# Performance work log

Measured on AMD Instinct MI355X. Metric: run time of the kernel, lower is better.

The kernel has to match this reference:

```python
import jax, jax.numpy as jnp
import numpy as np


def setup_inputs() -> dict:
    key = jax.random.key(0)
    k1, k2, k3 = jax.random.split(key, 3)
    B, H, S, D = 2, 16, 2048, 64
    q = jax.random.normal(k1, (B, H, S, D), dtype=jnp.float32)
    k = jax.random.normal(k2, (B, H, S, D), dtype=jnp.float32)
    v = jax.random.normal(k3, (B, H, S, D), dtype=jnp.float32)
    return {"q": q, "k": k, "v": v}


def reference(q, k, v):
    # q,k,v: [B,H,S,D]; causal attention with 1/sqrt(D) scaling, fp32 softmax.
    scale = 1.0 / (q.shape[-1] ** 0.5)
    scores = jnp.einsum('bhqd,bhkd->bhqk', q * scale, k)  # [B,H,S,S]
    S = scores.shape[-1]
    causal_mask = jnp.triu(jnp.ones((S, S), dtype=bool), k=1)
    scores = jnp.where(causal_mask, -jnp.inf, scores)
    attn = jax.nn.softmax(scores.astype(jnp.float32), axis=-1).astype(q.dtype)
    output = jnp.einsum('bhqk,bhkd->bhqd', attn, v)
    # Module also returns an all-zeros attn_weights placeholder of shape [B,H,S,S]
    attn_weights = jnp.zeros(scores.shape, dtype=q.dtype)
    return (output, attn_weights)
```

## Files before the change

### kernel.cpp

```cpp
#include <hip/hip_runtime.h>


typedef __bf16 bf16x8 __attribute__((ext_vector_type(8)));
typedef float f32x4 __attribute__((ext_vector_type(4)));

#define LOG2E 1.44269504088896340736f

__device__ __forceinline__ unsigned short f2bf(float f) {
  unsigned int u = __float_as_uint(f);
  u += 0x7fffu + ((u >> 16) & 1u);
  return (unsigned short)(u >> 16);
}

__device__ __forceinline__ void block_sync_lds() {
  asm volatile("s_waitcnt lgkmcnt(0)" ::: "memory");
  __builtin_amdgcn_s_barrier();
}

__device__ __forceinline__ float redmax_q(float x) {
  float a = x, b = x;
  asm volatile("" : "+v"(b));
  asm("v_permlane16_swap_b32 %0, %1" : "+v"(a), "+v"(b));
  float m = fmaxf(a, b);
  float c = m, d = m;
  asm volatile("" : "+v"(d));
  asm("v_permlane32_swap_b32 %0, %1" : "+v"(c), "+v"(d));
  return fmaxf(c, d);
}
__device__ __forceinline__ float redsum_q(float x) {
  float a = x, b = x;
  asm volatile("" : "+v"(b));
  asm("v_permlane16_swap_b32 %0, %1" : "+v"(a), "+v"(b));
  float s = a + b;
  float c = s, d = s;
  asm volatile("" : "+v"(d));
  asm("v_permlane32_swap_b32 %0, %1" : "+v"(c), "+v"(d));
  return c + d;
}

constexpr int Sdim = 2048, Ddim = 64, BHn = 32;
constexpr int STiles = 16;
constexpr int LDK = 72;
constexpr int OUT0 = BHn * Sdim * Ddim;
constexpr size_t FILL_PER_BH = 1048576;

__device__ __forceinline__ int vswz_m(int d) { return ((d >> 2) ^ (d >> 5)) & 7; }
__device__ __forceinline__ int vrow(int d) { return (d & 56) | ((d ^ (d >> 3)) & 7); }

__global__ __launch_bounds__(256, 2)
void flash_causal_kernel(const float* __restrict__ Q, const float* __restrict__ K,
                         const float* __restrict__ V, float* __restrict__ out) {
  __shared__ unsigned short Klds[2][64 * LDK];
  __shared__ unsigned short Vlds[2][64 * LDK];
  __shared__ unsigned short Plds[4][2][16 * LDK];

  const int tid  = threadIdx.x;
  const int wave = tid >> 6;
  const int lane = tid & 63;
  const int quad = lane >> 4;
  const int l15  = lane & 15;

  const int bh = blockIdx.x & (BHn - 1);
  const int g  = (int)(blockIdx.x >> 5);
  const int s  = (g & 1) ? (STiles - 1) - (g >> 1) : (g >> 1);
  const int jmax = 2 * s + 1;

  const int base  = bh * Sdim * Ddim;
  const int qbase = s * 128;

  bf16x8 aq[2][2];
  #pragma unroll
  for (int f = 0; f < 2; ++f) {
    const float* qp = Q + base + (qbase + 64 * f + wave * 16 + l15) * Ddim + quad * 8;
    #pragma unroll
    for (int s2 = 0; s2 < 2; ++s2) {
      float4 a = *(const float4*)(qp + 32 * s2);
      float4 b = *(const float4*)(qp + 32 * s2 + 4);
      union { unsigned short u[8]; bf16x8 v; } u;
      u.u[0] = f2bf(a.x * 0.125f); u.u[1] = f2bf(a.y * 0.125f);
      u.u[2] = f2bf(a.z * 0.125f); u.u[3] = f2bf(a.w * 0.125f);
      u.u[4] = f2bf(b.x * 0.125f); u.u[5] = f2bf(b.y * 0.125f);
      u.u[6] = f2bf(b.z * 0.125f); u.u[7] = f2bf(b.w * 0.125f);
      aq[f][s2] = u.v;
    }
  }

  f32x4 ot[2][4];
  #pragma unroll
  for (int f = 0; f < 2; ++f)
    #pragma unroll
    for (int t = 0; t < 4; ++t) ot[f][t] = (f32x4){0.f, 0.f, 0.f, 0.f};
  float mrun[2] = {-__builtin_inff(), -__builtin_inff()};
  float lrun[2] = {0.f, 0.f};

  const float4* kg4 = (const float4*)(K + base);
  const float4* vg4 = (const float4*)(V + base);
  float4 kf[4], vf[4];

  auto ldtile = [&](int j) {
    const float4* kp = kg4 + j * 1024;
    const float4* vp = vg4 + j * 1024;
    #pragma unroll
    for (int i = 0; i < 4; ++i) { kf[i] = kp[i * 256 + tid]; vf[i] = vp[i * 256 + tid]; }
  };
  auto stage = [&](int buf) {
    #pragma unroll
    for (int i = 0; i < 4; ++i) {
      int lin = i * 256 + tid;
      int row = lin >> 4;
      int c4  = (lin & 15) << 2;
      uint2 t2;
      t2.x = (unsigned int)f2bf(kf[i].x) | ((unsigned int)f2bf(kf[i].y) << 16);
      t2.y = (unsigned int)f2bf(kf[i].z) | ((unsigned int)f2bf(kf[i].w) << 16);
      *(uint2*)&Klds[buf][row * LDK + c4] = t2;
      const int sw = vswz_m(c4) << 3;
      Vlds[buf][vrow(c4 + 0) * LDK + (row ^ sw)] = f2bf(vf[i].x);
      Vlds[buf][vrow(c4 + 1) * LDK + (row ^ sw)] = f2bf(vf[i].y);
      Vlds[buf][vrow(c4 + 2) * LDK + (row ^ sw)] = f2bf(vf[i].z);
      Vlds[buf][vrow(c4 + 3) * LDK + (row ^ sw)] = f2bf(vf[i].w);
    }
  };

  ldtile(0); stage(0); ldtile(1);

  for (int j = 0; j <= jmax; ++j) {
    block_sync_lds();
    if (j < jmax) stage((j + 1) & 1);
    if (j + 2 <= jmax) ldtile(j + 2);

    const unsigned short* Kb = Klds[j & 1];
    const unsigned short* Vb = Vlds[j & 1];
    const bool f0act = (j <= 2 * s);

    f32x4 sc[2][4];
    #pragma unroll
    for (int f = 0; f < 2; ++f)
      #pragma unroll
      for (int t = 0; t < 4; ++t) sc[f][t] = (f32x4){0.f, 0.f, 0.f, 0.f};
    __builtin_amdgcn_s_setprio(1);
    #pragma unroll
    for (int s2 = 0; s2 < 2; ++s2) {
      #pragma unroll
      for (int t = 0; t < 4; ++t) {
        bf16x8 ka = *(const bf16x8*)&Kb[(16 * t + l15) * LDK + 32 * s2 + quad * 8];
        sc[0][t] = __builtin_amdgcn_mfma_f32_16x16x32_bf16(ka, aq[0][s2], sc[0][t], 0, 0, 0);
        sc[1][t] = __builtin_amdgcn_mfma_f32_16x16x32_bf16(ka, aq[1][s2], sc[1][t], 0, 0, 0);
      }
    }
    __builtin_amdgcn_s_setprio(0);

    #pragma unroll
    for (int f = 0; f < 2; ++f) {
      if (j == 2 * s + f) {
        const int qml = wave * 16 + l15;
        #pragma unroll
        for (int t = 0; t < 4; ++t)
          #pragma unroll
          for (int r = 0; r < 4; ++r)
            if (16 * t + 4 * quad + r > qml) sc[f][t][r] = -__builtin_inff();
      }
    }

    #pragma unroll
    for (int f = 0; f < 2; ++f) {
      if (f == 0 && !f0act) continue;
      float tmx[4];
      #pragma unroll
      for (int t = 0; t < 4; ++t)
        tmx[t] = fmaxf(fmaxf(sc[f][t][0], sc[f][t][1]),
                       fmaxf(sc[f][t][2], sc[f][t][3]));
      float mx = fmaxf(fmaxf(tmx[0], tmx[1]), fmaxf(tmx[2], tmx[3]));
      mx = redmax_q(mx);
      float mn    = fmaxf(mrun[f], mx);
      float alpha = __builtin_amdgcn_exp2f((mrun[f] - mn) * LOG2E);
      float msc   = mn * LOG2E;
      mrun[f] = mn;
      float rsp[4];
      #pragma unroll
      for (int t = 0; t < 4; ++t) {
        float p0 = __builtin_amdgcn_exp2f(fmaf(sc[f][t][0], LOG2E, -msc));
        float p1 = __builtin_amdgcn_exp2f(fmaf(sc[f][t][1], LOG2E, -msc));
        float p2 = __builtin_amdgcn_exp2f(fmaf(sc[f][t][2], LOG2E, -msc));
        float p3 = __builtin_amdgcn_exp2f(fmaf(sc[f][t][3], LOG2E, -msc));
        sc[f][t][0] = p0; sc[f][t][1] = p1; sc[f][t][2] = p2; sc[f][t][3] = p3;
        rsp[t] = (p0 + p1) + (p2 + p3);
      }
      float rs = (rsp[0] + rsp[1]) + (rsp[2] + rsp[3]);
      rs = redsum_q(rs);
      lrun[f] = lrun[f] * alpha + rs;
      #pragma unroll
      for (int t = 0; t < 4; ++t) {
        uint2 pw;
        pw.x = (unsigned int)f2bf(sc[f][t][0]) | ((unsigned int)f2bf(sc[f][t][1]) << 16);
        pw.y = (unsigned int)f2bf(sc[f][t][2]) | ((unsigned int)f2bf(sc[f][t][3]) << 16);
        *(uint2*)&Plds[wave][f][l15 * LDK + 16 * t + 4 * quad] = pw;
      }
      #pragma unroll
      for (int t = 0; t < 4; ++t)
        #pragma unroll
        for (int r = 0; r < 4; ++r) ot[f][t][r] *= alpha;
    }

    __builtin_amdgcn_s_setprio(1);
    #pragma unroll
    for (int s2 = 0; s2 < 2; ++s2) {
      bf16x8 pb0, pb1;
      if (f0act) pb0 = *(const bf16x8*)&Plds[wave][0][l15 * LDK + 32 * s2 + quad * 8];
      pb1 = *(const bf16x8*)&Plds[wave][1][l15 * LDK + 32 * s2 + quad * 8];
      #pragma unroll
      for (int t = 0; t < 4; ++t) {
        const int d = 16 * t + l15;
        bf16x8 va = *(const bf16x8*)&Vb[vrow(d) * LDK + (((4 * s2 + quad) ^ vswz_m(d)) << 3)];
        if (f0act)
          ot[0][t] = __builtin_amdgcn_mfma_f32_16x16x32_bf16(va, pb0, ot[0][t], 0, 0, 0);
        ot[1][t] = __builtin_amdgcn_mfma_f32_16x16x32_bf16(va, pb1, ot[1][t], 0, 0, 0);
      }
    }
    __builtin_amdgcn_s_setprio(0);
  }

  #pragma unroll
  for (int f = 0; f < 2; ++f) {
    float inv = 1.0f / lrun[f];
    float* orow = out + base + (qbase + 64 * f + wave * 16 + l15) * Ddim + 4 * quad;
    #pragma unroll
    for (int t = 0; t < 4; ++t) {
      f32x4 o4;
      o4.x = ot[f][t][0] * inv; o4.y = ot[f][t][1] * inv;
      o4.z = ot[f][t][2] * inv; o4.w = ot[f][t][3] * inv;
      *(f32x4*)(orow + 16 * t) = o4;
    }
  }

  {
    const int gp = (STiles - 1) - s;
    const int w  = 2 * gp + 1;
    const size_t start_f4 = (size_t)bh * FILL_PER_BH + (size_t)4096 * (gp * gp);
    const size_t count_f4 = (size_t)4096 * w;
    f32x4 z4 = (f32x4){0.f, 0.f, 0.f, 0.f};
    f32x4* zp = (f32x4*)(out + OUT0) + start_f4;
    for (size_t i = tid; i < count_f4; i += 256)
      __builtin_nontemporal_store(z4, zp + i);
  }
}

extern "C" void kernel_launch(void* const* d_in, const int* in_sizes, int n_in,
                              void* d_out, int out_size, void* d_ws, size_t ws_size,
                              hipStream_t stream) {
  const float* q = (const float*)d_in[0];
  const float* k = (const float*)d_in[1];
  const float* v = (const float*)d_in[2];
  float* out = (float*)d_out;
  dim3 grid(BHn * STiles);
  flash_causal_kernel<<<grid, dim3(256), 0, stream>>>(q, k, v, out);
}
```

Before: 585.4 us.

## Move zero-fill into dedicated blocks and shrink LDS padding for higher occupancy

Compute blocks no longer write their slice of the all-zeros attention-weight output at the end. Instead, 1024 extra blocks are appended to the grid, each writing a fixed contiguous chunk of zeros with nontemporal stores. This balances the large memory-bound fill independently of the uneven causal compute work. The LDS row stride drops from 72 to 68 halves and launch bounds go to 3 blocks per CU, so more blocks can be resident. The new stride may misalign 16-byte LDS vector reads and change the bank-conflict pattern.

```diff
diff --git a/kernel.cpp b/kernel.cpp
--- a/kernel.cpp
+++ b/kernel.cpp
@@ -40,28 +40,42 @@
 
 constexpr int Sdim = 2048, Ddim = 64, BHn = 32;
 constexpr int STiles = 16;
-constexpr int LDK = 72;
+constexpr int LDA = 68;
 constexpr int OUT0 = BHn * Sdim * Ddim;
-constexpr size_t FILL_PER_BH = 1048576;
+constexpr int NCOMPUTE = BHn * STiles;
+constexpr int NFILL = 1024;
+constexpr size_t FILL_F4_PER_BLK = 32768;
 
 __device__ __forceinline__ int vswz_m(int d) { return ((d >> 2) ^ (d >> 5)) & 7; }
 __device__ __forceinline__ int vrow(int d) { return (d & 56) | ((d ^ (d >> 3)) & 7); }
 
-__global__ __launch_bounds__(256, 2)
+__global__ __launch_bounds__(256, 3)
 void flash_causal_kernel(const float* __restrict__ Q, const float* __restrict__ K,
                          const float* __restrict__ V, float* __restrict__ out) {
-  __shared__ unsigned short Klds[2][64 * LDK];
-  __shared__ unsigned short Vlds[2][64 * LDK];
-  __shared__ unsigned short Plds[4][2][16 * LDK];
-
-  const int tid  = threadIdx.x;
+  __shared__ unsigned short Klds[2][64 * LDA];
+  __shared__ unsigned short Vlds[2][64 * LDA];
+  __shared__ unsigned short Plds[4][2][16 * LDA];
+
+  const int tid = threadIdx.x;
+  const int b   = (int)blockIdx.x;
+
+  if (b >= NCOMPUTE) {
+    const int fidx = b - NCOMPUTE;
+    f32x4* zp = (f32x4*)(out + OUT0) + (size_t)fidx * FILL_F4_PER_BLK;
+    const f32x4 z4 = (f32x4){0.f, 0.f, 0.f, 0.f};
+    #pragma unroll 4
+    for (size_t i = tid; i < FILL_F4_PER_BLK; i += 256)
+      __builtin_nontemporal_store(z4, zp + i);
+    return;
+  }
+
   const int wave = tid >> 6;
   const int lane = tid & 63;
   const int quad = lane >> 4;
   const int l15  = lane & 15;
 
-  const int bh = blockIdx.x & (BHn - 1);
-  const int g  = (int)(blockIdx.x >> 5);
+  const int bh = b & (BHn - 1);
+  const int g  = b >> 5;
   const int s  = (g & 1) ? (STiles - 1) - (g >> 1) : (g >> 1);
   const int jmax = 2 * s + 1;
 
@@ -75,12 +89,12 @@
     #pragma unroll
     for (int s2 = 0; s2 < 2; ++s2) {
       float4 a = *(const float4*)(qp + 32 * s2);
-      float4 b = *(const float4*)(qp + 32 * s2 + 4);
+      float4 bq = *(const float4*)(qp + 32 * s2 + 4);
       union { unsigned short u[8]; bf16x8 v; } u;
-      u.u[0] = f2bf(a.x * 0.125f); u.u[1] = f2bf(a.y * 0.125f);
-      u.u[2] = f2bf(a.z * 0.125f); u.u[3] = f2bf(a.w * 0.125f);
-      u.u[4] = f2bf(b.x * 0.125f); u.u[5] = f2bf(b.y * 0.125f);
-      u.u[6] = f2bf(b.z * 0.125f); u.u[7] = f2bf(b.w * 0.125f);
+      u.u[0] = f2bf(a.x * 0.125f);  u.u[1] = f2bf(a.y * 0.125f);
+      u.u[2] = f2bf(a.z * 0.125f);  u.u[3] = f2bf(a.w * 0.125f);
+      u.u[4] = f2bf(bq.x * 0.125f); u.u[5] = f2bf(bq.y * 0.125f);
+      u.u[6] = f2bf(bq.z * 0.125f); u.u[7] = f2bf(bq.w * 0.125f);
       aq[f][s2] = u.v;
     }
   }
@@ -112,12 +126,12 @@
       uint2 t2;
       t2.x = (unsigned int)f2bf(kf[i].x) | ((unsigned int)f2bf(kf[i].y) << 16);
       t2.y = (unsigned int)f2bf(kf[i].z) | ((unsigned int)f2bf(kf[i].w) << 16);
-      *(uint2*)&Klds[buf][row * LDK + c4] = t2;
+      *(uint2*)&Klds[buf][row * LDA + c4] = t2;
       const int sw = vswz_m(c4) << 3;
-      Vlds[buf][vrow(c4 + 0) * LDK + (row ^ sw)] = f2bf(vf[i].x);
-      Vlds[buf][vrow(c4 + 1) * LDK + (row ^ sw)] = f2bf(vf[i].y);
-      Vlds[buf][vrow(c4 + 2) * LDK + (row ^ sw)] = f2bf(vf[i].z);
-      Vlds[buf][vrow(c4 + 3) * LDK + (row ^ sw)] = f2bf(vf[i].w);
+      Vlds[buf][vrow(c4 + 0) * LDA + (row ^ sw)] = f2bf(vf[i].x);
+      Vlds[buf][vrow(c4 + 1) * LDA + (row ^ sw)] = f2bf(vf[i].y);
+      Vlds[buf][vrow(c4 + 2) * LDA + (row ^ sw)] = f2bf(vf[i].z);
+      Vlds[buf][vrow(c4 + 3) * LDA + (row ^ sw)] = f2bf(vf[i].w);
     }
   };
 
@@ -142,7 +156,7 @@
     for (int s2 = 0; s2 < 2; ++s2) {
       #pragma unroll
       for (int t = 0; t < 4; ++t) {
-        bf16x8 ka = *(const bf16x8*)&Kb[(16 * t + l15) * LDK + 32 * s2 + quad * 8];
+        bf16x8 ka = *(const bf16x8*)&Kb[(16 * t + l15) * LDA + 32 * s2 + quad * 8];
         sc[0][t] = __builtin_amdgcn_mfma_f32_16x16x32_bf16(ka, aq[0][s2], sc[0][t], 0, 0, 0);
         sc[1][t] = __builtin_amdgcn_mfma_f32_16x16x32_bf16(ka, aq[1][s2], sc[1][t], 0, 0, 0);
       }
@@ -193,7 +207,7 @@
         uint2 pw;
         pw.x = (unsigned int)f2bf(sc[f][t][0]) | ((unsigned int)f2bf(sc[f][t][1]) << 16);
         pw.y = (unsigned int)f2bf(sc[f][t][2]) | ((unsigned int)f2bf(sc[f][t][3]) << 16);
-        *(uint2*)&Plds[wave][f][l15 * LDK + 16 * t + 4 * quad] = pw;
+        *(uint2*)&Plds[wave][f][l15 * LDA + 16 * t + 4 * quad] = pw;
       }
       #pragma unroll
       for (int t = 0; t < 4; ++t)
@@ -205,12 +219,12 @@
     #pragma unroll
     for (int s2 = 0; s2 < 2; ++s2) {
       bf16x8 pb0, pb1;
-      if (f0act) pb0 = *(const bf16x8*)&Plds[wave][0][l15 * LDK + 32 * s2 + quad * 8];
-      pb1 = *(const bf16x8*)&Plds[wave][1][l15 * LDK + 32 * s2 + quad * 8];
+      if (f0act) pb0 = *(const bf16x8*)&Plds[wave][0][l15 * LDA + 32 * s2 + quad * 8];
+      pb1 = *(const bf16x8*)&Plds[wave][1][l15 * LDA + 32 * s2 + quad * 8];
       #pragma unroll
       for (int t = 0; t < 4; ++t) {
         const int d = 16 * t + l15;
-        bf16x8 va = *(const bf16x8*)&Vb[vrow(d) * LDK + (((4 * s2 + quad) ^ vswz_m(d)) << 3)];
+        bf16x8 va = *(const bf16x8*)&Vb[vrow(d) * LDA + (((4 * s2 + quad) ^ vswz_m(d)) << 3)];
         if (f0act)
           ot[0][t] = __builtin_amdgcn_mfma_f32_16x16x32_bf16(va, pb0, ot[0][t], 0, 0, 0);
         ot[1][t] = __builtin_amdgcn_mfma_f32_16x16x32_bf16(va, pb1, ot[1][t], 0, 0, 0);
@@ -230,17 +244,6 @@
       o4.z = ot[f][t][2] * inv; o4.w = ot[f][t][3] * inv;
       *(f32x4*)(orow + 16 * t) = o4;
     }
-  }
-
-  {
-    const int gp = (STiles - 1) - s;
-    const int w  = 2 * gp + 1;
-    const size_t start_f4 = (size_t)bh * FILL_PER_BH + (size_t)4096 * (gp * gp);
-    const size_t count_f4 = (size_t)4096 * w;
-    f32x4 z4 = (f32x4){0.f, 0.f, 0.f, 0.f};
-    f32x4* zp = (f32x4*)(out + OUT0) + start_f4;
-    for (size_t i = tid; i < count_f4; i += 256)
-      __builtin_nontemporal_store(z4, zp + i);
   }
 }
 
@@ -251,6 +254,6 @@
   const float* k = (const float*)d_in[1];
   const float* v = (const float*)d_in[2];
   float* out = (float*)d_out;
-  dim3 grid(BHn * STiles);
+  dim3 grid(NCOMPUTE + NFILL);
   flash_causal_kernel<<<grid, dim3(256), 0, stream>>>(q, k, v, out);
 }
```

After: 612.4 us. +4.6%, slower.
